# Kernel tuning notes

Hardware: AMD Instinct MI355X
Metric: run time of the kernel (lower is better)

Reference implementation:

```python
import jax, jax.numpy as jnp
import numpy as np

B, S, D_IN, D_H, D_OUT, N_LAYERS = 16, 2048, 512, 1024, 10, 2


def setup_inputs() -> dict:
    key = jax.random.key(0)
    ks = jax.random.split(key, 12)
    s = lambda fan_in: 1.0 / np.sqrt(fan_in)
    return {
        "input_vec": jax.random.normal(ks[0], (B, S, D_IN), jnp.float32),
        "game_vector": jax.random.normal(ks[1], (B, N_LAYERS, D_H), jnp.float32),
        "user_vector": jax.random.normal(ks[2], (B, N_LAYERS, D_H), jnp.float32),
        # input_fc: Linear(D_IN, 2*D_IN) -> ReLU -> Linear(2*D_IN, D_H) -> ReLU
        "W1": jax.random.uniform(ks[3], (D_IN, 2 * D_IN), jnp.float32, -s(D_IN), s(D_IN)),
        "b1": jnp.zeros((2 * D_IN,), jnp.float32),
        "W2": jax.random.uniform(ks[4], (2 * D_IN, D_H), jnp.float32, -s(2 * D_IN), s(2 * D_IN)),
        "b2": jnp.zeros((D_H,), jnp.float32),
        # output_fc: Linear(D_H, D_H//2) -> ReLU -> Linear(D_H//2, D_OUT) -> LogSoftmax
        "W3": jax.random.uniform(ks[5], (D_H, D_H // 2), jnp.float32, -s(D_H), s(D_H)),
        "b3": jnp.zeros((D_H // 2,), jnp.float32),
        "W4": jax.random.uniform(ks[6], (D_H // 2, D_OUT), jnp.float32, -s(D_H // 2), s(D_H // 2)),
        "b4": jnp.zeros((D_OUT,), jnp.float32),
    }


def _causal_attention(h):
    # unscaled causal self-attention: softmax(h h^T + triu(-inf)) h
    scores = jnp.einsum("bsd,btd->bst", h, h)  # [B,S,S]
    seq = h.shape[1]
    causal = jnp.tril(jnp.ones((seq, seq), dtype=bool))
    scores = jnp.where(causal[None], scores, -jnp.inf)
    attn = jax.nn.softmax(scores, axis=-1)
    return jnp.einsum("bst,btd->bsd", attn, h)


def reference(input_vec, game_vector, user_vector, W1, b1, W2, b2, W3, b3, W4, b4):
    h = jax.nn.relu(input_vec @ W1 + b1)  # dropout is identity in eval
    h = jax.nn.relu(h @ W2 + b2)          # [B,S,D_H]
    ctx = _causal_attention(h)
    o = jax.nn.relu(ctx @ W3 + b3)
    out = jax.nn.log_softmax(o @ W4 + b4, axis=-1)
    return out, game_vector, user_vector
```

## Files before the change

kernel.cpp:

```cpp
#include <hip/hip_runtime.h>
#include <stdint.h>

#define B_   16
#define S_   2048
#define DIN  512
#define DH   1024
#define DOUT 10

typedef unsigned short u16;
typedef unsigned int   u32;

typedef __bf16 bf16_t;
typedef bf16_t bf16x8 __attribute__((ext_vector_type(8)));
typedef float  f32x4  __attribute__((ext_vector_type(4)));

#define MASKVAL (-3.0e4f)
#define PZ_U16 ((size_t)160 * 16384)

__device__ __forceinline__ float b2f(u16 u) {
    union { u32 i; float f; } v; v.i = ((u32)u) << 16; return v.f;
}
__device__ __forceinline__ u16 f2b(float f) {
    union { float f; u32 i; } v; v.f = f;
    u32 u = v.i;
    u32 r = (u + 0x7FFFu + ((u >> 16) & 1u)) >> 16;
    return (u16)r;
}
__device__ __forceinline__ u32 pack2(float a, float b) {
    return (u32)f2b(a) | ((u32)f2b(b) << 16);
}

__device__ __forceinline__ f32x4 mfma16(bf16x8 a, bf16x8 b, f32x4 c) {
    return __builtin_amdgcn_mfma_f32_16x16x32_bf16(a, b, c, 0, 0, 0);
}

__device__ __forceinline__ void load_lds16(const u16* g, u16* l) {
    __builtin_amdgcn_global_load_lds(
        (__attribute__((address_space(1))) u32*)(g),
        (__attribute__((address_space(3))) u32*)(l), 16, 0, 0);
}

template<bool F32>
__device__ __forceinline__ uint4 ld8(const void* base, size_t eidx) {
    if constexpr (F32) {
        const float* p = (const float*)base + eidx;
        float4 f0 = *(const float4*)p;
        float4 f1 = *(const float4*)(p + 4);
        uint4 r;
        r.x = pack2(f0.x, f0.y); r.y = pack2(f0.z, f0.w);
        r.z = pack2(f1.x, f1.y); r.w = pack2(f1.z, f1.w);
        return r;
    } else {
        return *(const uint4*)((const u16*)base + eidx);
    }
}

__global__ __launch_bounds__(256) void prep_all(
    const float* __restrict__ x, u16* __restrict__ xb,
    const float* __restrict__ W1, const float* __restrict__ W2,
    const float* __restrict__ W3,
    u16* __restrict__ W1t, u16* __restrict__ W2t, u16* __restrict__ W3t)
{
    const int tid = threadIdx.x;
    if (blockIdx.x < 8192) {
        size_t e = ((size_t)blockIdx.x * 256 + tid) * 8;
        float4 f0 = *(const float4*)(x + e);
        float4 f1 = *(const float4*)(x + e + 4);
        uint4 r;
        r.x = pack2(f0.x, f0.y); r.y = pack2(f0.z, f0.w);
        r.z = pack2(f1.x, f1.y); r.w = pack2(f1.z, f1.w);
        *(uint4*)(xb + e) = r;
        return;
    }
    __shared__ u16 t[32][33];
    int i = blockIdx.x - 8192;
    const float* in; u16* out; int R, C, xt;
    if (i < 512)       { in = W1; out = W1t; R = 512;  C = 1024; xt = 32; }
    else if (i < 1536) { in = W2; out = W2t; R = 1024; C = 1024; xt = 32; i -= 512; }
    else               { in = W3; out = W3t; R = 1024; C = 512;  xt = 16; i -= 1536; }
    const int c0 = (i % xt) * 32, r0 = (i / xt) * 32;
    const int tx = tid & 31, ty = tid >> 5;
#pragma unroll
    for (int k = 0; k < 4; ++k)
        t[ty + k * 8][tx] = f2b(in[(size_t)(r0 + ty + k * 8) * C + c0 + tx]);
    __syncthreads();
#pragma unroll
    for (int k = 0; k < 4; ++k)
        out[(size_t)(c0 + ty + k * 8) * R + r0 + tx] = t[tx][ty + k * 8];
}

__global__ __launch_bounds__(256) void wprep(
    const float* __restrict__ W1, const float* __restrict__ W2,
    const float* __restrict__ W3,
    u16* __restrict__ W1t, u16* __restrict__ W2t, u16* __restrict__ W3t)
{
    __shared__ u16 t[32][33];
    int i = blockIdx.x;
    const float* in; u16* out; int R, C, xt;
    if (i < 512)       { in = W1; out = W1t; R = 512;  C = 1024; xt = 32; }
    else if (i < 1536) { in = W2; out = W2t; R = 1024; C = 1024; xt = 32; i -= 512; }
    else               { in = W3; out = W3t; R = 1024; C = 512;  xt = 16; i -= 1536; }
    const int c0 = (i % xt) * 32, r0 = (i / xt) * 32;
    const int tx = threadIdx.x, ty = threadIdx.y;
#pragma unroll
    for (int k = 0; k < 4; ++k)
        t[ty + k * 8][tx] = f2b(in[(size_t)(r0 + ty + k * 8) * C + c0 + tx]);
    __syncthreads();
#pragma unroll
    for (int k = 0; k < 4; ++k)
        out[(size_t)(c0 + ty + k * 8) * R + r0 + tx] = t[tx][ty + k * 8];
}

template<int QR>
__device__ __forceinline__ void rda(bf16x8 (&a)[4][2], const u16* T,
                                    int arow, int quad) {
#pragma unroll
    for (int mf = 0; mf < 4; ++mf) {
        const int row = arow + QR * 64 + mf * 16;
        const int sw = row & 7;
#pragma unroll
        for (int ks = 0; ks < 2; ++ks)
            a[mf][ks] = *(const bf16x8*)(T + row * 64 + (((ks * 4 + quad) ^ sw) << 3));
    }
}

template<int QC>
__device__ __forceinline__ void rdb(bf16x8 (&b)[2][2], const u16* T,
                                    int brow, int quad) {
#pragma unroll
    for (int nf = 0; nf < 2; ++nf) {
        const int row = brow + QC * 128 + nf * 16;
        const int sw = row & 7;
#pragma unroll
        for (int ks = 0; ks < 2; ++ks)
            b[nf][ks] = *(const bf16x8*)(T + row * 64 + (((ks * 4 + quad) ^ sw) << 3));
    }
}

template<int QR, int QC>
__device__ __forceinline__ void mmq(f32x4 (&acc)[2][2][4][2],
                                    const bf16x8 (&a)[4][2],
                                    const bf16x8 (&b)[2][2]) {
#pragma unroll
    for (int ks = 0; ks < 2; ++ks)
#pragma unroll
        for (int mf = 0; mf < 4; ++mf)
#pragma unroll
            for (int nf = 0; nf < 2; ++nf)
                acc[QR][QC][mf][nf] = mfma16(a[mf][ks], b[nf][ks], acc[QR][QC][mf][nf]);
}

#define G8BAR()  __builtin_amdgcn_s_barrier()
#define G8LGKM() do { asm volatile("s_waitcnt lgkmcnt(0)" ::: "memory"); \
                      __builtin_amdgcn_sched_barrier(0); } while (0)
#define G8VMC4() asm volatile("s_waitcnt vmcnt(4)" ::: "memory")

#define G8_LOOP_BODY(NT_)                                                     \
    const int NI = (NT_) >> 1;                                                \
    for (int i = 0; i < NI; ++i) {                                            \
        const int t1 = 2 * i + 1, t2 = 2 * i + 2, t3 = 2 * i + 3;             \
        rda<0>(a, AS_[0], arow, quad); rdb<0>(b0r, BS_[0], brow, quad);       \
        STGB(1, 2, t1); STGB(1, 3, t1);                                       \
        G8BAR(); G8LGKM();                                                    \
        __builtin_amdgcn_s_setprio(1); mmq<0, 0>(acc, a, b0r);                \
        __builtin_amdgcn_s_setprio(0); G8BAR();                               \
        rdb<1>(b1r, BS_[0], brow, quad);                                      \
        STGA(1, 1, t1); STGA(1, 3, t1);                                       \
        G8BAR(); G8LGKM();                                                    \
        __builtin_amdgcn_s_setprio(1); mmq<0, 1>(acc, a, b1r);                \
        __builtin_amdgcn_s_setprio(0); G8BAR();                               \
        rda<1>(a, AS_[0], arow, quad);                                        \
        if (t2 < (NT_)) { STGA(0, 0, t2); STGA(0, 2, t2); }                   \
        G8BAR(); G8LGKM();                                                    \
        __builtin_amdgcn_s_setprio(1); mmq<1, 0>(acc, a, b0r);                \
        __builtin_amdgcn_s_setprio(0); G8BAR();                               \
        if (t2 < (NT_)) { STGB(0, 0, t2); STGB(0, 1, t2); }                   \
        G8BAR();                                                              \
        __builtin_amdgcn_s_setprio(1); mmq<1, 1>(acc, a, b1r);                \
        __builtin_amdgcn_s_setprio(0);                                        \
        G8VMC4(); G8BAR();                                                    \
        rda<0>(a, AS_[1], arow, quad); rdb<0>(b0r, BS_[1], brow, quad);       \
        if (t2 < (NT_)) { STGB(0, 2, t2); STGB(0, 3, t2); }                   \
        G8BAR(); G8LGKM();                                                    \
        __builtin_amdgcn_s_setprio(1); mmq<0, 0>(acc, a, b0r);                \
        __builtin_amdgcn_s_setprio(0); G8BAR();                               \
        rdb<1>(b1r, BS_[1], brow, quad);                                      \
        if (t2 < (NT_)) { STGA(0, 1, t2); STGA(0, 3, t2); }                   \
        G8BAR(); G8LGKM();                                                    \
        __builtin_amdgcn_s_setprio(1); mmq<0, 1>(acc, a, b1r);                \
        __builtin_amdgcn_s_setprio(0); G8BAR();                               \
        rda<1>(a, AS_[1], arow, quad);                                        \
        if (t3 < (NT_)) { STGA(1, 0, t3); STGA(1, 2, t3); }                   \
        G8BAR(); G8LGKM();                                                    \
        __builtin_amdgcn_s_setprio(1); mmq<1, 0>(acc, a, b0r);                \
        __builtin_amdgcn_s_setprio(0); G8BAR();                               \
        if (t3 < (NT_)) { STGB(1, 0, t3); STGB(1, 1, t3); }                   \
        G8BAR();                                                              \
        __builtin_amdgcn_s_setprio(1); mmq<1, 1>(acc, a, b1r);                \
        __builtin_amdgcn_s_setprio(0);                                        \
        G8VMC4(); G8BAR();                                                    \
    }

#define G8_SETUP()                                                            \
    const int tid  = threadIdx.x;                                             \
    const int lane = tid & 63;                                                \
    const int w    = tid >> 6;                                                \
    const int wm   = w >> 2, wn = w & 3;                                      \
    const int quad = lane >> 4, l15 = lane & 15;                              \
    const int rg = tid >> 3;                                                  \
    const int ch = (lane & 7) ^ ((lane >> 3) & 7);                            \
    const int wslot = w * 512;                                                \
    f32x4 acc[2][2][4][2];                                                    \
    _Pragma("unroll") for (int p_ = 0; p_ < 2; ++p_)                          \
    _Pragma("unroll") for (int q_ = 0; q_ < 2; ++q_)                          \
    _Pragma("unroll") for (int m_ = 0; m_ < 4; ++m_)                          \
    _Pragma("unroll") for (int n_ = 0; n_ < 2; ++n_)                          \
        acc[p_][q_][m_][n_] = (f32x4){0.f, 0.f, 0.f, 0.f};                    \
    bf16x8 a[4][2], b0r[2][2], b1r[2][2];                                     \
    const int arow = wm * 128 + l15;                                          \
    const int brow = wn * 32 + l15;

#define G8_PROLOGUE()                                                         \
    STGA(0, 0, 0); STGA(0, 1, 0); STGA(0, 2, 0); STGA(0, 3, 0);               \
    STGB(0, 0, 0); STGB(0, 1, 0); STGB(0, 2, 0); STGB(0, 3, 0);               \
    STGA(1, 0, 1); STGA(1, 2, 1);                                             \
    STGB(1, 0, 1); STGB(1, 1, 1);                                             \
    G8VMC4(); G8BAR();

__global__ __launch_bounds__(512, 2) void gemm8(
    const u16* __restrict__ A, const u16* __restrict__ Bt,
    const float* __restrict__ bias, u16* __restrict__ C,
    int N, int K, int do_relu)
{
    __shared__ __attribute__((aligned(16))) u16 AS_[2][16384];
    __shared__ __attribute__((aligned(16))) u16 BS_[2][16384];

    G8_SETUP()
    const int m0 = blockIdx.x * 256, n0 = blockIdx.y * 256;
    const u16* gA = A  + (size_t)(m0 + rg) * K + ch * 8;
    const u16* gB = Bt + (size_t)(n0 + rg) * K + ch * 8;

#define STGA(BUF, U, T) load_lds16(gA + (size_t)(U) * 64 * K + (T) * 64, \
                                   &AS_[BUF][(U) * 4096 + wslot])
#define STGB(BUF, U, T) load_lds16(gB + (size_t)(U) * 64 * K + (T) * 64, \
                                   &BS_[BUF][(U) * 4096 + wslot])

    const int NT = K >> 6;
    G8_PROLOGUE()
    G8_LOOP_BODY(NT)
#undef STGA
#undef STGB

    const int r0 = quad * 4;
#pragma unroll
    for (int qc = 0; qc < 2; ++qc)
#pragma unroll
    for (int nf = 0; nf < 2; ++nf) {
        const int col = n0 + qc * 128 + wn * 32 + nf * 16 + l15;
        const float bv = bias[col];
#pragma unroll
        for (int qr = 0; qr < 2; ++qr)
#pragma unroll
        for (int mf = 0; mf < 4; ++mf) {
            const int rowb = m0 + wm * 128 + qr * 64 + mf * 16 + r0;
#pragma unroll
            for (int r = 0; r < 4; ++r) {
                float v = acc[qr][qc][mf][nf][r] + bv;
                if (do_relu) v = fmaxf(v, 0.f);
                C[(size_t)(rowb + r) * N + col] = f2b(v);
            }
        }
    }
}

__global__ __launch_bounds__(512, 2) void score8(
    const u16* __restrict__ h, u16* __restrict__ P, int nbb)
{
    __shared__ __attribute__((aligned(16))) u16 AS_[2][16384];
    __shared__ __attribute__((aligned(16))) u16 BS_[2][16384];

    int z, t;
    if ((nbb & 7) == 0) {
        const int xcd = blockIdx.x & 7, slot = blockIdx.x >> 3;
        z = (slot / 36) * 8 + xcd;
        t = slot % 36;
    } else {
        z = blockIdx.x / 36;
        t = blockIdx.x % 36;
    }

    int bi = 0;
    while ((bi + 1) * (bi + 2) / 2 <= t) ++bi;
    const int bj = t - bi * (bi + 1) / 2;
    const bool diag = (bi == bj);

    G8_SETUP()
    const int m0 = bi * 256, n0 = bj * 256;
    const u16* hz = h + (size_t)z * S_ * DH;
    const u16* gA = hz + (size_t)(m0 + rg) * DH + ch * 8;
    const u16* gB = hz + (size_t)(n0 + rg) * DH + ch * 8;

#define STGA(BUF, U, T) load_lds16(gA + (size_t)(U) * 64 * DH + (T) * 64, \
                                   &AS_[BUF][(U) * 4096 + wslot])
#define STGB(BUF, U, T) load_lds16(gB + (size_t)(U) * 64 * DH + (T) * 64, \
                                   &BS_[BUF][(U) * 4096 + wslot])

    const int NT = DH >> 6;
    G8_PROLOGUE()
    G8_LOOP_BODY(NT)
#undef STGA
#undef STGB

    const int mi = 2 * bi + wm;
    const int g  = mi >> 2;
    u16* Pz = P + (size_t)z * PZ_U16
                + (size_t)(4 * (g + 1) * (mi - 2 * g)) * 16384;
    const size_t rstride = (size_t)(4 * (g + 1)) * 128;

    const int r0 = quad * 4;
#pragma unroll
    for (int qc = 0; qc < 2; ++qc) {
        const int ni = 2 * bj + qc;
#pragma unroll
        for (int nf = 0; nf < 2; ++nf) {
            const int cl = wn * 32 + nf * 16 + l15;
            const int colg = n0 + qc * 128 + cl;
#pragma unroll
            for (int qr = 0; qr < 2; ++qr)
#pragma unroll
            for (int mf = 0; mf < 4; ++mf) {
                const int rl = qr * 64 + mf * 16 + r0;
                const int rowg = m0 + wm * 128 + rl;
#pragma unroll
                for (int r = 0; r < 4; ++r) {
                    float v = acc[qr][qc][mf][nf][r];
                    if (diag && colg > rowg + r) v = MASKVAL;
                    Pz[(size_t)(rl + r) * rstride + ni * 128 + cl] = f2b(v);
                }
            }
        }
    }
}

__global__ __launch_bounds__(512, 2) void pv8(
    const u16* __restrict__ P, const u16* __restrict__ hT,
    u16* __restrict__ ctx, int nb)
{
    __shared__ __attribute__((aligned(16))) u16 AS_[2][16384];
    __shared__ __attribute__((aligned(16))) u16 BS_[2][16384];

    const int per_bi = 4 * nb;
    const int bi  = 7 - (int)(blockIdx.x / per_bi);
    const int rem = blockIdx.x % per_bi;
    const int nj  = rem & 3;
    const int z   = rem >> 2;

    const int g  = bi >> 1;
    const int K  = (g + 1) * 512;
    const int NT = K >> 6;
    const int n0 = nj * 256;

    const u16* Az = P + (size_t)z * PZ_U16
                      + (size_t)(4 * (g + 1) * (2 * bi - 2 * g)) * 16384;
    const u16* Bz = hT + (size_t)z * DH * S_;
    u16*       C  = ctx + (size_t)z * S_ * DH;

    G8_SETUP()
    const u16* gA = Az + (size_t)rg * K + ch * 8;
    const u16* gB = Bz + (size_t)(n0 + rg) * S_ + ch * 8;

#define STGA(BUF, U, T) load_lds16(gA + (size_t)(U) * 64 * K + (T) * 64, \
                                   &AS_[BUF][(U) * 4096 + wslot])
#define STGB(BUF, U, T) load_lds16(gB + (size_t)(U) * 64 * S_ + (T) * 64, \
                                   &BS_[BUF][(U) * 4096 + wslot])

    G8_PROLOGUE()
    G8_LOOP_BODY(NT)
#undef STGA
#undef STGB

    const int r0 = quad * 4;
#pragma unroll
    for (int qc = 0; qc < 2; ++qc)
#pragma unroll
    for (int nf = 0; nf < 2; ++nf) {
        const int col = n0 + qc * 128 + wn * 32 + nf * 16 + l15;
#pragma unroll
        for (int qr = 0; qr < 2; ++qr)
#pragma unroll
        for (int mf = 0; mf < 4; ++mf) {
            const int rowb = bi * 256 + wm * 128 + qr * 64 + mf * 16 + r0;
#pragma unroll
            for (int r = 0; r < 4; ++r)
                C[(size_t)(rowb + r) * DH + col] = f2b(acc[qr][qc][mf][nf][r]);
        }
    }
}

__global__ __launch_bounds__(256) void score_a(
    const u16* __restrict__ h, u16* __restrict__ P)
{
    __shared__ __attribute__((aligned(16))) u16 As[128 * 32];
    __shared__ __attribute__((aligned(16))) u16 Bs[128 * 32];

    const int mi = 15 - blockIdx.x;
    const int ni = blockIdx.y;
    const int g  = mi >> 2;
    const int r4 = (g + 1) * 4;
    if (ni >= r4) return;

    const int tid = threadIdx.x;
    u16* Pz = P + (size_t)blockIdx.z * PZ_U16
                + (size_t)(4 * (g + 1) * (mi - 2 * g)) * 16384;
    const size_t rstride = (size_t)r4 * 128;

    if (ni > mi) {
        const u16 mb = f2b(MASKVAL);
        const u32 m2 = (u32)mb | ((u32)mb << 16);
        uint4 mv; mv.x = m2; mv.y = m2; mv.z = m2; mv.w = m2;
#pragma unroll
        for (int i = 0; i < 8; ++i) {
            int q = tid + i * 256;
            int row = q >> 4, cl = (q & 15) * 8;
            *(uint4*)&Pz[(size_t)row * rstride + ni * 128 + cl] = mv;
        }
        return;
    }

    const int m0 = mi * 128, n0 = ni * 128;
    const u16* A = h + (size_t)blockIdx.z * S_ * DH;

    const int lane = tid & 63;
    const int w    = tid >> 6;
    const int wm   = w >> 1, wn = w & 1;
    const int quad = lane >> 4, l15 = lane & 15;

    const int c0 = tid, c1 = tid + 256;
    const u16* gA0 = A + ((size_t)(m0 + (c0 >> 2)) * DH + (c0 & 3) * 8);
    const u16* gA1 = A + ((size_t)(m0 + (c1 >> 2)) * DH + (c1 & 3) * 8);
    const u16* gB0 = A + ((size_t)(n0 + (c0 >> 2)) * DH + (c0 & 3) * 8);
    const u16* gB1 = A + ((size_t)(n0 + (c1 >> 2)) * DH + (c1 & 3) * 8);
    u16* lA0 = &As[(w * 64) * 8];
    u16* lA1 = &As[(256 + w * 64) * 8];
    u16* lB0 = &Bs[(w * 64) * 8];
    u16* lB1 = &Bs[(256 + w * 64) * 8];

    f32x4 acc[4][4];
#pragma unroll
    for (int i = 0; i < 4; ++i)
#pragma unroll
        for (int j = 0; j < 4; ++j) acc[i][j] = (f32x4){0.f, 0.f, 0.f, 0.f};

    const int nk = DH >> 5;
    for (int kk = 0; kk < nk; ++kk) {
        load_lds16(gA0, lA0); load_lds16(gA1, lA1);
        load_lds16(gB0, lB0); load_lds16(gB1, lB1);
        gA0 += 32; gA1 += 32; gB0 += 32; gB1 += 32;
        __syncthreads();
        bf16x8 af[4], bfr[4];
#pragma unroll
        for (int i = 0; i < 4; ++i)
            af[i] = *(const bf16x8*)&As[(wm * 64 + i * 16 + l15) * 32 + quad * 8];
#pragma unroll
        for (int j = 0; j < 4; ++j)
            bfr[j] = *(const bf16x8*)&Bs[(wn * 64 + j * 16 + l15) * 32 + quad * 8];
#pragma unroll
        for (int i = 0; i < 4; ++i)
#pragma unroll
            for (int j = 0; j < 4; ++j)
                acc[i][j] = mfma16(af[i], bfr[j], acc[i][j]);
        __syncthreads();
    }

    const int r0 = quad * 4;
#pragma unroll
    for (int j = 0; j < 4; ++j) {
        int cl = wn * 64 + j * 16 + l15;
#pragma unroll
        for (int i = 0; i < 4; ++i) {
            int rl = wm * 64 + i * 16 + r0;
#pragma unroll
            for (int r = 0; r < 4; ++r) {
                int row = rl + r;
                float v = (n0 + cl <= m0 + row) ? acc[i][j][r] : MASKVAL;
                Pz[(size_t)row * rstride + ni * 128 + cl] = f2b(v);
            }
        }
    }
}

__global__ __launch_bounds__(256) void softmax_rows(u16* __restrict__ P)
{
    const int tid = threadIdx.x;
    const int lane = tid & 63, w = tid >> 6;
    const int quad = lane >> 4;
    const size_t row = (size_t)blockIdx.x * 4 + w;
    const int z    = (int)(row >> 11);
    const int rloc = (int)(row & (S_ - 1));
    const int mi = rloc >> 7, g = mi >> 2;
    const int kb = g + 1;
    u16* p = P + (size_t)z * PZ_U16
               + (size_t)(4 * (g + 1) * (mi - 2 * g)) * 16384
               + (size_t)(rloc & 127) * ((g + 1) * 4 * 128);
    float v[32];
    float m = -1e30f;
    for (int k = 0; k < kb; ++k) {
        if (k * 4 + quad <= mi) {
            uint4 u = *(const uint4*)&p[k * 512 + lane * 8];
            const u32* uu = (const u32*)&u;
#pragma unroll
            for (int i = 0; i < 4; ++i) {
                float a = b2f((u16)(uu[i] & 0xFFFFu));
                float b = b2f((u16)(uu[i] >> 16));
                v[k * 8 + 2 * i] = a; v[k * 8 + 2 * i + 1] = b;
                m = fmaxf(m, fmaxf(a, b));
            }
        } else {
#pragma unroll
            for (int i = 0; i < 8; ++i) v[k * 8 + i] = MASKVAL;
        }
    }
#pragma unroll
    for (int off = 32; off >= 1; off >>= 1) m = fmaxf(m, __shfl_xor(m, off, 64));
    float s = 0.f;
    for (int k = 0; k < kb; ++k)
#pragma unroll
        for (int i = 0; i < 8; ++i) {
            float e = __expf(v[k * 8 + i] - m);
            v[k * 8 + i] = e; s += e;
        }
#pragma unroll
    for (int off = 32; off >= 1; off >>= 1) s += __shfl_xor(s, off, 64);
    float inv = 1.0f / s;
    for (int k = 0; k < kb; ++k) {
        uint4 u; u32* uu = (u32*)&u;
#pragma unroll
        for (int i = 0; i < 4; ++i)
            uu[i] = pack2(v[k * 8 + 2 * i] * inv, v[k * 8 + 2 * i + 1] * inv);
        *(uint4*)&p[k * 512 + lane * 8] = u;
    }
}

__global__ __launch_bounds__(256) void pv_a(
    const u16* __restrict__ P, const u16* __restrict__ hT, u16* __restrict__ ctx,
    int nb)
{
    __shared__ __attribute__((aligned(16))) u16 As[128 * 32];
    __shared__ __attribute__((aligned(16))) u16 Bs[128 * 32];

    const int idx = blockIdx.x;
    const int per_mi = 8 * nb;
    const int mi = 15 - (idx / per_mi);
    const int sub = idx % per_mi;
    const int nblk = sub & 7;
    const int z    = sub >> 3;
    const int g = mi >> 2;
    const int m0 = mi * 128;
    const int n0 = nblk * 128;
    const size_t rstride = (size_t)((g + 1) * 4) * 128;
    const u16* A  = P  + (size_t)z * PZ_U16
                       + (size_t)(4 * (g + 1) * (mi - 2 * g)) * 16384;
    const u16* Bt = hT + (size_t)z * DH * S_;
    u16*      C   = ctx + (size_t)z * S_ * DH;

    const int tid  = threadIdx.x;
    const int lane = tid & 63;
    const int w    = tid >> 6;
    const int wm   = w >> 1, wn = w & 1;
    const int quad = lane >> 4, l15 = lane & 15;

    const int c0 = tid, c1 = tid + 256;
    const u16* gA0 = A  + ((size_t)(c0 >> 2) * rstride + (c0 & 3) * 8);
    const u16* gA1 = A  + ((size_t)(c1 >> 2) * rstride + (c1 & 3) * 8);
    const u16* gB0 = Bt + ((size_t)(n0 + (c0 >> 2)) * S_ + (c0 & 3) * 8);
    const u16* gB1 = Bt + ((size_t)(n0 + (c1 >> 2)) * S_ + (c1 & 3) * 8);
    u16* lA0 = &As[(w * 64) * 8];
    u16* lA1 = &As[(256 + w * 64) * 8];
    u16* lB0 = &Bs[(w * 64) * 8];
    u16* lB1 = &Bs[(256 + w * 64) * 8];

    f32x4 acc[4][4];
#pragma unroll
    for (int i = 0; i < 4; ++i)
#pragma unroll
        for (int j = 0; j < 4; ++j) acc[i][j] = (f32x4){0.f, 0.f, 0.f, 0.f};

    const int nk = (mi + 1) * 4;
    for (int kk = 0; kk < nk; ++kk) {
        load_lds16(gA0, lA0); load_lds16(gA1, lA1);
        load_lds16(gB0, lB0); load_lds16(gB1, lB1);
        gA0 += 32; gA1 += 32; gB0 += 32; gB1 += 32;
        __syncthreads();
        bf16x8 af[4], bfr[4];
#pragma unroll
        for (int i = 0; i < 4; ++i)
            af[i] = *(const bf16x8*)&As[(wm * 64 + i * 16 + l15) * 32 + quad * 8];
#pragma unroll
        for (int j = 0; j < 4; ++j)
            bfr[j] = *(const bf16x8*)&Bs[(wn * 64 + j * 16 + l15) * 32 + quad * 8];
#pragma unroll
        for (int i = 0; i < 4; ++i)
#pragma unroll
            for (int j = 0; j < 4; ++j)
                acc[i][j] = mfma16(af[i], bfr[j], acc[i][j]);
        __syncthreads();
    }

    const int r0 = quad * 4;
#pragma unroll
    for (int j = 0; j < 4; ++j) {
        int col = n0 + wn * 64 + j * 16 + l15;
#pragma unroll
        for (int i = 0; i < 4; ++i) {
            int rowb = m0 + wm * 64 + i * 16 + r0;
#pragma unroll
            for (int r = 0; r < 4; ++r)
                C[(size_t)(rowb + r) * DH + col] = f2b(acc[i][j][r]);
        }
    }
}

template<bool AF32>
__global__ __launch_bounds__(256) void gemm_bt_bias_relu(
    const void* __restrict__ A, const u16* __restrict__ Bt,
    const float* __restrict__ bias, u16* __restrict__ C,
    int M, int N, int K, int do_relu)
{
    __shared__ __attribute__((aligned(16))) u16 As[128 * 32];
    __shared__ __attribute__((aligned(16))) u16 Bs[128 * 32];

    const int tid  = threadIdx.x;
    const int lane = tid & 63;
    const int w    = tid >> 6;
    const int wm   = w >> 1, wn = w & 1;
    const int quad = lane >> 4, l15 = lane & 15;

    const int m0 = blockIdx.x * 128;
    const int n0 = blockIdx.y * 128;

    const int c0 = tid, c1 = tid + 256;
    size_t eA0 = (size_t)(m0 + (c0 >> 2)) * K + (c0 & 3) * 8;
    size_t eA1 = (size_t)(m0 + (c1 >> 2)) * K + (c1 & 3) * 8;
    size_t eB0 = (size_t)(n0 + (c0 >> 2)) * K + (c0 & 3) * 8;
    size_t eB1 = (size_t)(n0 + (c1 >> 2)) * K + (c1 & 3) * 8;

    f32x4 acc[4][4];
#pragma unroll
    for (int i = 0; i < 4; ++i)
#pragma unroll
        for (int j = 0; j < 4; ++j) acc[i][j] = (f32x4){0.f, 0.f, 0.f, 0.f};

    uint4 va0 = ld8<AF32>(A, eA0), va1 = ld8<AF32>(A, eA1);
    uint4 vb0 = ld8<false>(Bt, eB0), vb1 = ld8<false>(Bt, eB1);

    const int nk = K >> 5;
    for (int kk = 0; kk < nk; ++kk) {
        __syncthreads();
        *(uint4*)&As[c0 * 8] = va0;
        *(uint4*)&As[c1 * 8] = va1;
        *(uint4*)&Bs[c0 * 8] = vb0;
        *(uint4*)&Bs[c1 * 8] = vb1;
        if (kk + 1 < nk) {
            eA0 += 32; eA1 += 32; eB0 += 32; eB1 += 32;
            va0 = ld8<AF32>(A, eA0); va1 = ld8<AF32>(A, eA1);
            vb0 = ld8<false>(Bt, eB0); vb1 = ld8<false>(Bt, eB1);
        }
        __syncthreads();
        bf16x8 af[4], bfr[4];
#pragma unroll
        for (int i = 0; i < 4; ++i)
            af[i] = *(const bf16x8*)&As[(wm * 64 + i * 16 + l15) * 32 + quad * 8];
#pragma unroll
        for (int j = 0; j < 4; ++j)
            bfr[j] = *(const bf16x8*)&Bs[(wn * 64 + j * 16 + l15) * 32 + quad * 8];
#pragma unroll
        for (int i = 0; i < 4; ++i)
#pragma unroll
            for (int j = 0; j < 4; ++j)
                acc[i][j] = mfma16(af[i], bfr[j], acc[i][j]);
    }

    const int r0 = quad * 4;
#pragma unroll
    for (int j = 0; j < 4; ++j) {
        int col = n0 + wn * 64 + j * 16 + l15;
        float bv = bias[col];
#pragma unroll
        for (int i = 0; i < 4; ++i) {
            int rowb = m0 + wm * 64 + i * 16 + r0;
#pragma unroll
            for (int r = 0; r < 4; ++r) {
                float v = acc[i][j][r] + bv;
                if (do_relu) v = fmaxf(v, 0.f);
                C[(size_t)(rowb + r) * N + col] = f2b(v);
            }
        }
    }
}

__global__ __launch_bounds__(256) void transpose_v(
    const u16* __restrict__ in, u16* __restrict__ out, int R, int C)
{
    __shared__ u16 st[64][33];
    const u16* ip = in  + (size_t)blockIdx.z * R * C;
    u16*       op = out + (size_t)blockIdx.z * R * C;
    const int c0 = blockIdx.x * 64, r0 = blockIdx.y * 32;
    const int t = threadIdx.x;
    {
        const int row = t >> 3, ch = t & 7;
        uint4 v = *(const uint4*)&ip[(size_t)(r0 + row) * C + c0 + ch * 8];
        const u16* pv = (const u16*)&v;
#pragma unroll
        for (int k = 0; k < 8; ++k) st[ch * 8 + k][row] = pv[k];
    }
    __syncthreads();
    {
        const int oc = t >> 2, r4 = t & 3;
        uint4 v; u16* pv = (u16*)&v;
#pragma unroll
        for (int k = 0; k < 8; ++k) pv[k] = st[oc][r4 * 8 + k];
        *(uint4*)&op[(size_t)(c0 + oc) * R + r0 + r4 * 8] = v;
    }
}

__global__ __launch_bounds__(256) void head_logsoftmax(
    const u16* __restrict__ o, const float* __restrict__ W4,
    const float* __restrict__ b4, float* __restrict__ out)
{
    __shared__ float W4s[DIN * DOUT];
    __shared__ float b4s[DOUT];
    const int tid = threadIdx.x;
    for (int i = tid; i < DIN * DOUT; i += 256) W4s[i] = W4[i];
    if (tid < DOUT) b4s[tid] = b4[tid];
    __syncthreads();
    const int lane = tid & 63, w = tid >> 6;
    for (int rr = 0; rr < 4; ++rr) {
        const size_t row = (size_t)blockIdx.x * 16 + w * 4 + rr;
        const uint4 ov = *(const uint4*)&o[row * DIN + lane * 8];
        const u32* ou = (const u32*)&ov;
        float oc[8];
#pragma unroll
        for (int i = 0; i < 4; ++i) {
            oc[2*i]   = b2f((u16)(ou[i] & 0xFFFFu));
            oc[2*i+1] = b2f((u16)(ou[i] >> 16));
        }
        float acc[DOUT];
#pragma unroll
        for (int c = 0; c < DOUT; ++c) acc[c] = 0.f;
#pragma unroll
        for (int i = 0; i < 8; ++i) {
            int k = lane * 8 + i;
            float x = oc[i];
#pragma unroll
            for (int c = 0; c < DOUT; ++c) acc[c] += x * W4s[k * DOUT + c];
        }
#pragma unroll
        for (int off = 32; off >= 1; off >>= 1)
#pragma unroll
            for (int c = 0; c < DOUT; ++c) acc[c] += __shfl_xor(acc[c], off, 64);
        float mx = -1e30f;
#pragma unroll
        for (int c = 0; c < DOUT; ++c) { acc[c] += b4s[c]; mx = fmaxf(mx, acc[c]); }
        float sum = 0.f;
#pragma unroll
        for (int c = 0; c < DOUT; ++c) sum += __expf(acc[c] - mx);
        float lse = mx + logf(sum);
        if (lane == 0) {
#pragma unroll
            for (int c = 0; c < DOUT; ++c) out[row * DOUT + c] = acc[c] - lse;
        }
    }
}

extern "C" void kernel_launch(void* const* d_in, const int* in_sizes, int n_in,
                              void* d_out, int out_size, void* d_ws, size_t ws_size,
                              hipStream_t stream) {
    const float* x  = (const float*)d_in[0];
    const float* gv = (const float*)d_in[1];
    const float* uv = (const float*)d_in[2];
    const float* W1 = (const float*)d_in[3];
    const float* b1 = (const float*)d_in[4];
    const float* W2 = (const float*)d_in[5];
    const float* b2 = (const float*)d_in[6];
    const float* W3 = (const float*)d_in[7];
    const float* b3 = (const float*)d_in[8];
    const float* W4 = (const float*)d_in[9];
    const float* b4 = (const float*)d_in[10];
    float* out = (float*)d_out;

    char* ws = (char*)d_ws;
    const size_t MB64 = (size_t)67108864;
    const size_t MiB  = (size_t)1048576;
    const size_t TIER_A3 = 2 * MB64 + 80 * MiB + 4 * MiB;
    const size_t TIER_A2 = 2 * MB64 + 72 * MiB + 8 * MiB;
    const size_t TIER_B  = 3 * MB64 + 5 * MiB;

    if (ws_size >= TIER_A3) {
        u16* h1  = (u16*)(ws);
        u16* hT  = h1;
        u16* h   = (u16*)(ws + MB64);
        u16* ctx = h;
        u16* xb  = (u16*)(ws + 2 * MB64);
        u16* P   = xb;
        u16* o   = xb;
        u16* W1t = (u16*)(ws + 2 * MB64 + 80 * MiB);
        u16* W2t = W1t + 512 * 1024;
        u16* W3t = W2t + 1024 * 1024;

        prep_all<<<10240, 256, 0, stream>>>(x, xb, W1, W2, W3, W1t, W2t, W3t);
        gemm8<<<dim3(128, 4), 512, 0, stream>>>(xb, W1t, b1, h1, 1024, 512, 1);
        gemm8<<<dim3(128, 4), 512, 0, stream>>>(h1, W2t, b2, h,  1024, 1024, 1);

        transpose_v<<<dim3(16, 64, 16), 256, 0, stream>>>(h, hT, 2048, 1024);
        score8<<<36 * 16, 512, 0, stream>>>(h, P, 16);
        softmax_rows<<<8192, 256, 0, stream>>>(P);
        pv8<<<32 * 16, 512, 0, stream>>>(P, hT, ctx, 16);

        gemm8<<<dim3(128, 2), 512, 0, stream>>>(ctx, W3t, b3, o, 512, 1024, 1);
        head_logsoftmax<<<2048, 256, 0, stream>>>(o, W4, b4, out);
    } else if (ws_size >= TIER_A2) {
        u16* h1   = (u16*)(ws);
        u16* ctx  = h1;
        u16* h    = (u16*)(ws + MB64);
        u16* o    = h;
        u16* xb   = (u16*)(ws + 2 * MB64);
        u16* hT_c = xb;
        u16* P_c  = (u16*)(ws + 2 * MB64 + 32 * MiB);
        u16* W1t  = (u16*)(ws + 2 * MB64 + 72 * MiB);
        u16* W2t  = W1t + 512 * 1024;
        u16* W3t  = W2t + 1024 * 1024;

        prep_all<<<10240, 256, 0, stream>>>(x, xb, W1, W2, W3, W1t, W2t, W3t);
        gemm8<<<dim3(128, 4), 512, 0, stream>>>(xb, W1t, b1, h1, 1024, 512, 1);
        gemm8<<<dim3(128, 4), 512, 0, stream>>>(h1, W2t, b2, h,  1024, 1024, 1);

        for (int c = 0; c < 2; ++c) {
            const u16* hc  = h   + (size_t)c * 8 * S_ * DH;
            u16*       cxc = ctx + (size_t)c * 8 * S_ * DH;
            transpose_v<<<dim3(16, 64, 8), 256, 0, stream>>>(hc, hT_c, 2048, 1024);
            score8<<<36 * 8, 512, 0, stream>>>(hc, P_c, 8);
            softmax_rows<<<4096, 256, 0, stream>>>(P_c);
            pv_a<<<16 * 8 * 8, 256, 0, stream>>>(P_c, hT_c, cxc, 8);
        }

        gemm8<<<dim3(128, 2), 512, 0, stream>>>(ctx, W3t, b3, o, 512, 1024, 1);
        head_logsoftmax<<<2048, 256, 0, stream>>>(o, W4, b4, out);
    } else if (ws_size >= TIER_B) {
        u16* h1   = (u16*)(ws);
        u16* ctx  = h1;
        u16* h    = (u16*)(ws + MB64);
        u16* xb   = (u16*)(ws + 2 * MB64);
        u16* hT_c = xb;
        u16* P_c  = (u16*)(ws + 2 * MB64 + 16 * MiB);
        u16* o    = (u16*)(ws + 2 * MB64);
        u16* W1t  = (u16*)(ws + 3 * MB64);
        u16* W2t  = W1t + 512 * 1024;
        u16* W3t  = W2t + 1024 * 1024;

        prep_all<<<10240, 256, 0, stream>>>(x, xb, W1, W2, W3, W1t, W2t, W3t);
        gemm8<<<dim3(128, 4), 512, 0, stream>>>(xb, W1t, b1, h1, 1024, 512, 1);
        gemm8<<<dim3(128, 4), 512, 0, stream>>>(h1, W2t, b2, h,  1024, 1024, 1);

        for (int c = 0; c < 4; ++c) {
            const u16* hc  = h   + (size_t)c * 4 * S_ * DH;
            u16*       cxc = ctx + (size_t)c * 4 * S_ * DH;
            transpose_v<<<dim3(16, 64, 4), 256, 0, stream>>>(hc, hT_c, 2048, 1024);
            score8<<<36 * 4, 512, 0, stream>>>(hc, P_c, 4);
            softmax_rows<<<2048, 256, 0, stream>>>(P_c);
            pv_a<<<16 * 8 * 4, 256, 0, stream>>>(P_c, hT_c, cxc, 4);
        }

        gemm8<<<dim3(128, 2), 512, 0, stream>>>(ctx, W3t, b3, o, 512, 1024, 1);
        head_logsoftmax<<<2048, 256, 0, stream>>>(o, W4, b4, out);
    } else {
        u16* h    = (u16*)(ws);
        u16* hT_b = (u16*)(ws + MB64);
        u16* P_b  = (u16*)(ws + MB64 + 4 * MiB);
        u16* ctx_b= (u16*)(ws + MB64 + 12 * MiB);
        u16* o_b  = (u16*)(ws + MB64 + 16 * MiB);
        u16* W1t  = (u16*)(ws + MB64 + 18 * MiB);
        u16* W2t  = W1t + 512 * 1024;
        u16* W3t  = W2t + 1024 * 1024;
        u16* h1_b = P_b;

        wprep<<<2048, dim3(32, 8), 0, stream>>>(W1, W2, W3, W1t, W2t, W3t);

        for (int c = 0; c < 8; ++c) {
            const float* xc = x + (size_t)c * 4096 * DIN;
            u16*         hc = h + (size_t)c * 4096 * DH;
            gemm_bt_bias_relu<true ><<<dim3(32, 8), 256, 0, stream>>>(xc, W1t, b1, h1_b,
                                                                      4096, 1024, 512, 1);
            gemm_bt_bias_relu<false><<<dim3(32, 8), 256, 0, stream>>>(h1_b, W2t, b2, hc,
                                                                      4096, 1024, 1024, 1);
        }
        for (int b = 0; b < B_; ++b) {
            const u16* hb = h + (size_t)b * S_ * DH;
            transpose_v<<<dim3(16, 64, 1), 256, 0, stream>>>(hb, hT_b, 2048, 1024);
            score_a<<<dim3(16, 16, 1), 256, 0, stream>>>(hb, P_b);
            softmax_rows<<<512, 256, 0, stream>>>(P_b);
            pv_a<<<16 * 8, 256, 0, stream>>>(P_b, hT_b, ctx_b, 1);
            gemm_bt_bias_relu<false><<<dim3(16, 4), 256, 0, stream>>>(ctx_b, W3t, b3, o_b,
                                                                      2048, 512, 1024, 1);
            head_logsoftmax<<<128, 256, 0, stream>>>(o_b, W4, b4,
                                                     out + (size_t)b * S_ * DOUT);
        }
    }

    size_t n_gv = (size_t)in_sizes[1], n_uv = (size_t)in_sizes[2];
    size_t o0 = (size_t)out_size - n_gv - n_uv;
    hipMemcpyAsync(out + o0,        gv, n_gv * 4, hipMemcpyDeviceToDevice, stream);
    hipMemcpyAsync(out + o0 + n_gv, uv, n_uv * 4, hipMemcpyDeviceToDevice, stream);
}
```

Measured before the change: 543.1 us.

## Fold h transpose into score kernel as extra blocks to overlap with QK^T

Removes the separate transpose_v launch and adds 128 extra blocks per batch to the score8 grid that transpose h into hT through LDS while the score blocks compute QK^T. The aim is to save one launch and let the memory-bound transpose run alongside the compute-bound score tiles. The transpose blocks use a padded shared-memory staging buffer. The cost is extra blocks competing for CUs, and a transpose path that is less tuned than the dedicated kernel. For nbb=16 the transpose blocks are scheduled after all score blocks, so there may be little real overlap.

New measurement: 537.4 us. Within noise of the previous version (-1.1%).

```diff
diff --git a/kernel.cpp b/kernel.cpp
--- a/kernel.cpp
+++ b/kernel.cpp
@@ -274,19 +274,54 @@
 }
 
 __global__ __launch_bounds__(512, 2) void score8(
-    const u16* __restrict__ h, u16* __restrict__ P, int nbb)
+    const u16* __restrict__ h, u16* __restrict__ P, u16* __restrict__ hT,
+    int nbb)
 {
     __shared__ __attribute__((aligned(16))) u16 AS_[2][16384];
     __shared__ __attribute__((aligned(16))) u16 BS_[2][16384];
 
-    int z, t;
+    int z, t = 0, r = 0;
+    bool isT = false;
     if ((nbb & 7) == 0) {
         const int xcd = blockIdx.x & 7, slot = blockIdx.x >> 3;
-        z = (slot / 36) * 8 + xcd;
-        t = slot % 36;
+        const int sth = (36 * nbb) >> 3;
+        if (slot < sth) { z = (slot / 36) * 8 + xcd; t = slot % 36; }
+        else { const int ql = slot - sth; z = (ql >> 7) * 8 + xcd; r = ql & 127; isT = true; }
     } else {
-        z = blockIdx.x / 36;
-        t = blockIdx.x % 36;
+        const int ns = 36 * nbb;
+        if ((int)blockIdx.x < ns) { z = blockIdx.x / 36; t = blockIdx.x % 36; }
+        else { const int q = blockIdx.x - ns; z = q >> 7; r = q & 127; isT = true; }
+    }
+
+    if (isT) {
+        const int cx = r & 15, ry0 = (r >> 4) * 8;
+        const u16* hz  = h  + (size_t)z * S_ * DH;
+        u16*       hTz = hT + (size_t)z * DH * S_;
+        const int th  = threadIdx.x;
+        const int sel = th >> 8, tt = th & 255;
+        u16* st = (u16*)AS_[0] + sel * 2112;
+#pragma unroll
+        for (int jj = 0; jj < 4; ++jj) {
+            const int ry = ry0 + 2 * jj + sel;
+            {
+                const int row = tt >> 3, chv = tt & 7;
+                uint4 v = *(const uint4*)&hz[(size_t)(ry * 32 + row) * DH
+                                             + cx * 64 + chv * 8];
+                const u16* pv = (const u16*)&v;
+#pragma unroll
+                for (int k = 0; k < 8; ++k) st[(chv * 8 + k) * 33 + row] = pv[k];
+            }
+            __syncthreads();
+            {
+                const int oc = tt >> 2, r4 = tt & 3;
+                uint4 v; u16* pv = (u16*)&v;
+#pragma unroll
+                for (int k = 0; k < 8; ++k) pv[k] = st[oc * 33 + r4 * 8 + k];
+                *(uint4*)&hTz[(size_t)(cx * 64 + oc) * S_ + ry * 32 + r4 * 8] = v;
+            }
+            __syncthreads();
+        }
+        return;
     }
 
     int bi = 0;
@@ -332,10 +367,10 @@
                 const int rl = qr * 64 + mf * 16 + r0;
                 const int rowg = m0 + wm * 128 + rl;
 #pragma unroll
-                for (int r = 0; r < 4; ++r) {
-                    float v = acc[qr][qc][mf][nf][r];
-                    if (diag && colg > rowg + r) v = MASKVAL;
-                    Pz[(size_t)(rl + r) * rstride + ni * 128 + cl] = f2b(v);
+                for (int rr = 0; rr < 4; ++rr) {
+                    float v = acc[qr][qc][mf][nf][rr];
+                    if (diag && colg > rowg + rr) v = MASKVAL;
+                    Pz[(size_t)(rl + rr) * rstride + ni * 128 + cl] = f2b(v);
                 }
             }
         }
@@ -811,8 +846,7 @@
         gemm8<<<dim3(128, 4), 512, 0, stream>>>(xb, W1t, b1, h1, 1024, 512, 1);
         gemm8<<<dim3(128, 4), 512, 0, stream>>>(h1, W2t, b2, h,  1024, 1024, 1);
 
-        transpose_v<<<dim3(16, 64, 16), 256, 0, stream>>>(h, hT, 2048, 1024);
-        score8<<<36 * 16, 512, 0, stream>>>(h, P, 16);
+        score8<<<(36 + 128) * 16, 512, 0, stream>>>(h, P, hT, 16);
         softmax_rows<<<8192, 256, 0, stream>>>(P);
         pv8<<<32 * 16, 512, 0, stream>>>(P, hT, ctx, 16);
 
@@ -837,8 +871,7 @@
         for (int c = 0; c < 2; ++c) {
             const u16* hc  = h   + (size_t)c * 8 * S_ * DH;
             u16*       cxc = ctx + (size_t)c * 8 * S_ * DH;
-            transpose_v<<<dim3(16, 64, 8), 256, 0, stream>>>(hc, hT_c, 2048, 1024);
-            score8<<<36 * 8, 512, 0, stream>>>(hc, P_c, 8);
+            score8<<<(36 + 128) * 8, 512, 0, stream>>>(hc, P_c, hT_c, 8);
             softmax_rows<<<4096, 256, 0, stream>>>(P_c);
             pv_a<<<16 * 8 * 8, 256, 0, stream>>>(P_c, hT_c, cxc, 8);
         }
@@ -864,8 +897,7 @@
         for (int c = 0; c < 4; ++c) {
             const u16* hc  = h   + (size_t)c * 4 * S_ * DH;
             u16*       cxc = ctx + (size_t)c * 4 * S_ * DH;
-            transpose_v<<<dim3(16, 64, 4), 256, 0, stream>>>(hc, hT_c, 2048, 1024);
-            score8<<<36 * 4, 512, 0, stream>>>(hc, P_c, 4);
+            score8<<<(36 + 128) * 4, 512, 0, stream>>>(hc, P_c, hT_c, 4);
             softmax_rows<<<2048, 256, 0, stream>>>(P_c);
             pv_a<<<16 * 8 * 4, 256, 0, stream>>>(P_c, hT_c, cxc, 4);
         }
```
